# Kernel optimization log

Measured on AMD Instinct MI355X. Metric: run time of the kernel, lower is better.

Reference implementation:

```python
import jax, jax.numpy as jnp
import numpy as np

B, T, C = 2, 2048, 2048
H = 16
ROPE_DIM, NOPE_DIM, V_DIM = 64, 64, 128
HEAD_DIM = NOPE_DIM + ROPE_DIM  # 128
Q_RANK, KV_RANK = 1536, 512


def setup_inputs() -> dict:
    key = jax.random.key(0)
    ks = jax.random.split(key, 8)
    std = 0.02
    return {
        "x": jax.random.normal(ks[0], (B, T, C), jnp.float32),
        "cos": jax.random.normal(ks[1], (1, T, 1, ROPE_DIM // 2), jnp.float32),
        "sin": jax.random.normal(ks[2], (1, T, 1, ROPE_DIM // 2), jnp.float32),
        "wq_down": jax.random.normal(ks[3], (Q_RANK, C), jnp.float32) * std,
        "wq_up": jax.random.normal(ks[4], (H * HEAD_DIM, Q_RANK), jnp.float32) * std,
        "wkv_down": jax.random.normal(ks[5], (KV_RANK, C), jnp.float32) * std,
        "wkv_up": jax.random.normal(ks[6], (H * (HEAD_DIM + V_DIM), KV_RANK), jnp.float32) * std,
        "wo": jax.random.normal(ks[7], (C, H * V_DIM), jnp.float32) * std,
    }


def _rope(x, cos, sin):
    # x: [B, T, H, rope_dim]
    d = x.shape[-1] // 2
    x1, x2 = x[..., :d], x[..., d:]
    return jnp.concatenate([x1 * cos + x2 * sin, -x1 * sin + x2 * cos], axis=-1)


def _rms_norm(x):
    eps = jnp.finfo(x.dtype).eps
    return x * jax.lax.rsqrt(jnp.mean(jnp.square(x), axis=-1, keepdims=True) + eps)


def reference(x, cos, sin, wq_down, wq_up, wkv_down, wkv_up, wo):
    # Low-rank q projection
    q = jnp.einsum('btc,rc,dr->btd', x, wq_down, wq_up)
    q = q.reshape(B, T, H, HEAD_DIM)
    q_nope, q_rope = q[..., :NOPE_DIM], q[..., NOPE_DIM:]
    # Low-rank kv projection (naive decompression)
    kv = jnp.einsum('btc,rc,dr->btd', x, wkv_down, wkv_up)
    kv = kv.reshape(B, T, H, HEAD_DIM + V_DIM)
    k_nope = kv[..., :NOPE_DIM]
    k_rope = kv[..., NOPE_DIM:HEAD_DIM]
    v = kv[..., HEAD_DIM:]
    # Partial RoPE on the rope sub-dims only
    q_rope = _rope(q_rope, cos, sin)
    k_rope = _rope(k_rope, cos, sin)
    q = _rms_norm(jnp.concatenate([q_nope, q_rope], axis=-1))
    k = _rms_norm(jnp.concatenate([k_nope, k_rope], axis=-1))
    # Causal SDPA: [B, H, T, T]
    scale = 1.0 / jnp.sqrt(jnp.float32(HEAD_DIM))
    scores = jnp.einsum('bthd,bshd->bhts', q, k) * scale
    causal = jnp.tril(jnp.ones((T, T), dtype=bool))
    scores = jnp.where(causal, scores, jnp.finfo(scores.dtype).min)
    probs = jax.nn.softmax(scores, axis=-1)
    y = jnp.einsum('bhts,bshd->bthd', probs, v).reshape(B, T, H * V_DIM)
    return y @ wo.T
```

## Files before the change

kernel.cpp:

```cpp
#include <hip/hip_runtime.h>
#include <hip/hip_bf16.h>
#include <math.h>
#include <type_traits>

#define AS1 __attribute__((address_space(1)))
#define AS3 __attribute__((address_space(3)))

typedef __bf16  bf16x8 __attribute__((ext_vector_type(8)));
typedef float   f32x4  __attribute__((ext_vector_type(4)));
typedef __hip_bfloat16 bf16;

#define MFMA16x16x32 __builtin_amdgcn_mfma_f32_16x16x32_bf16

__device__ __forceinline__ void gload16(const void* g, void* l) {
  __builtin_amdgcn_global_load_lds((const AS1 void*)g, (AS3 void*)l, 16, 0, 0);
}

__device__ __forceinline__ unsigned short bfbits(float v) {
  return __builtin_bit_cast(unsigned short, __float2bfloat16(v));
}

#define LGKM0 __asm__ volatile("s_waitcnt lgkmcnt(0)" ::: "memory")
#define BARRIER __builtin_amdgcn_s_barrier()
#define VMCNT(n) __asm__ volatile("s_waitcnt vmcnt(" #n ")" ::: "memory")

struct CastArgs {
  const float4* src[6];
  ushort4* dst[6];
  unsigned bound[6];
};

__global__ __launch_bounds__(256) void f2bf_multi(CastArgs a) {
  unsigned i = blockIdx.x * 256 + threadIdx.x;
  if (i >= a.bound[5]) return;
  unsigned lo = 0;
  int s = 0;
#pragma unroll
  for (int k = 0; k < 5; k++) {
    if (i >= a.bound[k]) { s = k + 1; lo = a.bound[k]; }
  }
  unsigned idx = i - lo;
  float4 v = a.src[s][idx];
  ushort4 o;
  o.x = bfbits(v.x); o.y = bfbits(v.y); o.z = bfbits(v.z); o.w = bfbits(v.w);
  a.dst[s][idx] = o;
}

template <typename OutT, bool KVUP>
__global__ __launch_bounds__(512, 2) void gemm8p(const bf16* __restrict__ A,
                                                 const bf16* __restrict__ W,
                                                 OutT* __restrict__ Cp,
                                                 bf16* __restrict__ vT,
                                                 int N, int K, int lda) {
  __shared__ __align__(16) char lds[131072];
  const int t = threadIdx.x, w = t >> 6, lane = t & 63;
  const int quad = lane >> 4, l16 = lane & 15;
  const int wr = w >> 2, wc = w & 3;
  const size_t m0 = (size_t)blockIdx.x * 256;
  const size_t n0 = (size_t)blockIdx.y * 256;
  const int NI = K >> 7;

  const int srow = w * 8 + (lane >> 3);
  const int schunk = (lane & 7) ^ ((lane >> 3) & 7);
  const bf16* aS = A + (m0 + srow) * (size_t)lda + schunk * 8;
  const bf16* bS = W + (n0 + srow) * (size_t)K + schunk * 8;

  auto stageA = [&](int kt, int h) {
    const bf16* src = aS + (size_t)(h * 128) * lda + kt * 64;
    char* dst = lds + (kt & 1) * 32768 + h * 16384 + w * 1024;
    gload16(src, dst);
    gload16(src + (size_t)64 * lda, dst + 8192);
  };
  auto stageB = [&](int kt, int h) {
    const bf16* src = bS + (size_t)(h * 128) * K + kt * 64;
    char* dst = lds + 65536 + (kt & 1) * 32768 + h * 16384 + w * 1024;
    gload16(src, dst);
    gload16(src + (size_t)64 * K, dst + 8192);
  };

  const int cq0 = ((quad) ^ (l16 & 7)) * 16;
  const int cq1 = ((4 + quad) ^ (l16 & 7)) * 16;
  const char* aRb = lds + wr * 16384 + l16 * 128;
  const char* bRb = lds + 65536 + (wc >> 1) * 16384 + ((wc & 1) * 64 + l16) * 128;
  auto rdA = [&](int sl, int mf, int kh) -> bf16x8 {
    return *(const bf16x8*)(aRb + sl * 32768 + mf * 2048 + (kh ? cq1 : cq0));
  };
  auto rdB = [&](int sl, int nf, int kh) -> bf16x8 {
    return *(const bf16x8*)(bRb + sl * 32768 + nf * 2048 + (kh ? cq1 : cq0));
  };

  bf16x8 aR[8][2], bR[4][2];
  f32x4 acc[8][4];
#pragma unroll
  for (int i = 0; i < 8; i++)
#pragma unroll
    for (int j = 0; j < 4; j++) acc[i][j] = f32x4{0.f, 0.f, 0.f, 0.f};

  auto cluster = [&](int mh, int nh) {
    __builtin_amdgcn_s_setprio(1);
#pragma unroll
    for (int m2 = 0; m2 < 4; ++m2)
#pragma unroll
      for (int n2 = 0; n2 < 2; ++n2)
#pragma unroll
        for (int kh = 0; kh < 2; ++kh)
          acc[mh * 4 + m2][nh * 2 + n2] =
              MFMA16x16x32(aR[mh * 4 + m2][kh], bR[nh * 2 + n2][kh],
                           acc[mh * 4 + m2][nh * 2 + n2], 0, 0, 0);
    __builtin_amdgcn_s_setprio(0);
  };

  stageA(0, 0); stageA(0, 1); stageB(0, 0); stageB(0, 1);
  stageA(1, 0); stageA(1, 1); stageB(1, 0); stageB(1, 1);
  VMCNT(8);
  BARRIER;
#pragma unroll
  for (int mf = 0; mf < 4; ++mf)
#pragma unroll
    for (int kh = 0; kh < 2; ++kh) aR[mf][kh] = rdA(0, mf, kh);
#pragma unroll
  for (int nf = 0; nf < 2; ++nf)
#pragma unroll
    for (int kh = 0; kh < 2; ++kh) bR[nf][kh] = rdB(0, nf, kh);

  for (int i = 0; i < NI; ++i) {
    const int kt1 = 2 * i + 1, kt2 = 2 * i + 2, kt3 = 2 * i + 3;
    const bool hn = (i + 1 < NI);

#pragma unroll
    for (int kh = 0; kh < 2; ++kh) { bR[2][kh] = rdB(0, 2, kh); bR[3][kh] = rdB(0, 3, kh); }
    if (i > 0) stageB(kt1, 0);
    BARRIER; LGKM0;
    cluster(0, 0);
    BARRIER;

#pragma unroll
    for (int mf = 0; mf < 4; ++mf)
#pragma unroll
      for (int kh = 0; kh < 2; ++kh) aR[4 + mf][kh] = rdA(0, 4 + mf, kh);
    if (i > 0) stageB(kt1, 1);
    BARRIER; LGKM0;
    cluster(0, 1);
    BARRIER;

    if (hn) stageA(kt2, 0);
    BARRIER; LGKM0;
    cluster(1, 0);
    if (hn) { VMCNT(2); } else { VMCNT(0); }
    BARRIER;

#pragma unroll
    for (int mf = 0; mf < 4; ++mf)
#pragma unroll
      for (int kh = 0; kh < 2; ++kh) aR[mf][kh] = rdA(1, mf, kh);
#pragma unroll
    for (int nf = 0; nf < 2; ++nf)
#pragma unroll
      for (int kh = 0; kh < 2; ++kh) bR[nf][kh] = rdB(1, nf, kh);
    if (hn) stageA(kt2, 1);
    BARRIER; LGKM0;
    cluster(1, 1);
    BARRIER;

#pragma unroll
    for (int kh = 0; kh < 2; ++kh) { bR[2][kh] = rdB(1, 2, kh); bR[3][kh] = rdB(1, 3, kh); }
    if (hn) stageB(kt2, 0);
    BARRIER; LGKM0;
    cluster(0, 0);
    BARRIER;

#pragma unroll
    for (int mf = 0; mf < 4; ++mf)
#pragma unroll
      for (int kh = 0; kh < 2; ++kh) aR[4 + mf][kh] = rdA(1, 4 + mf, kh);
    if (hn) stageB(kt2, 1);
    BARRIER; LGKM0;
    cluster(0, 1);
    BARRIER;

    if (hn) stageA(kt3, 0);
    BARRIER; LGKM0;
    cluster(1, 0);
    if (hn) { VMCNT(2); }
    BARRIER;

    if (hn) {
#pragma unroll
      for (int mf = 0; mf < 4; ++mf)
#pragma unroll
        for (int kh = 0; kh < 2; ++kh) aR[mf][kh] = rdA(0, mf, kh);
#pragma unroll
      for (int nf = 0; nf < 2; ++nf)
#pragma unroll
        for (int kh = 0; kh < 2; ++kh) bR[nf][kh] = rdB(0, nf, kh);
      stageA(kt3, 1);
    }
    BARRIER; LGKM0;
    cluster(1, 1);
    BARRIER;
  }

  if constexpr (!KVUP) {
#pragma unroll
    for (int mf = 0; mf < 8; ++mf)
#pragma unroll
      for (int nf = 0; nf < 4; ++nf)
#pragma unroll
        for (int r = 0; r < 4; ++r) {
          size_t row = m0 + wr * 128 + mf * 16 + quad * 4 + r;
          size_t col = n0 + wc * 64 + nf * 16 + l16;
          float v = acc[mf][nf][r];
          if constexpr (std::is_same<OutT, float>::value)
            Cp[row * N + col] = v;
          else
            Cp[row * N + col] = __float2bfloat16(v);
        }
  } else {
    const int head = (int)(n0 >> 8);
    if (wc < 2) {
#pragma unroll
      for (int mf = 0; mf < 8; ++mf)
#pragma unroll
        for (int nf = 0; nf < 4; ++nf)
#pragma unroll
          for (int r = 0; r < 4; ++r) {
            size_t row = m0 + wr * 128 + mf * 16 + quad * 4 + r;
            size_t col = n0 + wc * 64 + nf * 16 + l16;
            Cp[row * 4096 + col] = __float2bfloat16(acc[mf][nf][r]);
          }
    } else {
#pragma unroll
      for (int mf = 0; mf < 8; ++mf) {
        size_t row = m0 + wr * 128 + mf * 16 + quad * 4;
        int bb = (int)(row >> 11), tloc = (int)(row & 2047);
#pragma unroll
        for (int nf = 0; nf < 4; ++nf) {
          int d = (wc - 2) * 64 + nf * 16 + l16;
          ushort4 v4;
          v4.x = bfbits(acc[mf][nf][0]);
          v4.y = bfbits(acc[mf][nf][1]);
          v4.z = bfbits(acc[mf][nf][2]);
          v4.w = bfbits(acc[mf][nf][3]);
          *(ushort4*)(vT + ((size_t)(bb * 16 + head) * 128 + d) * 2048 + tloc) = v4;
        }
      }
    }
  }
}

__global__ __launch_bounds__(256) void rope_rms(const bf16* __restrict__ qraw,
                                                const bf16* __restrict__ kvraw,
                                                const float* __restrict__ cosp,
                                                const float* __restrict__ sinp,
                                                bf16* __restrict__ qn,
                                                bf16* __restrict__ kn) {
  const int bt = blockIdx.x;
  const int w = threadIdx.x >> 6, lane = threadIdx.x & 63;
  const int h = blockIdx.y * 4 + w;
  const int tt = bt & 2047;
  const float c = cosp[tt * 32 + (lane & 31)];
  const float s = sinp[tt * 32 + (lane & 31)];
  const float inv128 = 1.0f / 128.0f;
  const float eps = 1.1920929e-7f;

  {
    const bf16* base = qraw + (size_t)bt * 2048 + h * 128;
    float a = (float)base[lane];
    float o = (float)base[64 + lane];
    float partner = __shfl_xor(o, 32);
    float orope = (lane < 32) ? (o * c + partner * s) : (o * c - partner * s);
    float ss = a * a + orope * orope;
#pragma unroll
    for (int off = 1; off < 64; off <<= 1) ss += __shfl_xor(ss, off);
    float rn = rsqrtf(ss * inv128 + eps);
    bf16* outp = qn + ((size_t)bt * 16 + h) * 128;
    outp[lane] = __float2bfloat16(a * rn);
    outp[64 + lane] = __float2bfloat16(orope * rn);
  }
  {
    const bf16* base = kvraw + (size_t)bt * 4096 + h * 256;
    float a = (float)base[lane];
    float o = (float)base[64 + lane];
    float partner = __shfl_xor(o, 32);
    float orope = (lane < 32) ? (o * c + partner * s) : (o * c - partner * s);
    float ss = a * a + orope * orope;
#pragma unroll
    for (int off = 1; off < 64; off <<= 1) ss += __shfl_xor(ss, off);
    float rn = rsqrtf(ss * inv128 + eps);
    bf16* outp = kn + ((size_t)bt * 16 + h) * 128;
    outp[lane] = __float2bfloat16(a * rn);
    outp[64 + lane] = __float2bfloat16(orope * rn);
  }
}

__global__ __launch_bounds__(256, 2) void attn_kernel(const bf16* __restrict__ qn,
                                                      const bf16* __restrict__ kn,
                                                      const bf16* __restrict__ vT,
                                                      bf16* __restrict__ y) {
  __shared__ __align__(16) bf16 Ks[2 * 64 * 128];
  __shared__ __align__(16) bf16 Vs[2 * 128 * 64];
  __shared__ __align__(16) bf16 Ps[4 * 16 * 64];
  const int t = threadIdx.x, w = t >> 6, lane = t & 63;
  const int quad = lane >> 4, l16 = lane & 15;
  const int b = blockIdx.x >> 4, h = blockIdx.x & 15;
  const int pr = (int)blockIdx.y;
  const int T_ = 2048, H_ = 16;
  const float K1 = 0.08838834764831845f * 1.4426950408889634f;
  const float K2 = -12.0f * 1.4426950408889634f;

  const int cgk = l16 ^ ((w * 4 + quad) & 7);
  const char* kg0 = (const char*)(kn + ((size_t)(b * T_) * H_ + h) * 128)
                    + (size_t)(w * 4 + quad) * 4096 + (size_t)cgk * 16;
  const int vrow = w * 8 + (lane >> 3);
  const int cgv = (lane & 7) ^ (vrow & 7);
  const char* vg0 = (const char*)(vT + ((size_t)(b * H_ + h) * 128 + vrow) * T_)
                    + (size_t)cgv * 16;

  auto stage = [&](auto bufc, int it2) {
    constexpr int BUF = decltype(bufc)::value;
    const size_t koff = (size_t)it2 * 262144;
    const size_t voff = (size_t)it2 * 128;
#pragma unroll
    for (int is = 0; is < 4; ++is)
      gload16(kg0 + koff + (size_t)is * 65536,
              (char*)Ks + BUF * 16384 + is * 4096 + w * 1024);
#pragma unroll
    for (int is = 0; is < 4; ++is)
      gload16(vg0 + voff + (size_t)is * 131072,
              (char*)Vs + BUF * 16384 + is * 4096 + w * 1024);
  };

  auto body = [&](auto bufc, int it, int nt, int xb,
                  bf16x8* qf, f32x4* yacc, float* lrow) {
    constexpr int BUF = decltype(bufc)::value;
    if (it + 1 < nt) {
      stage(std::integral_constant<int, 1 - BUF>{}, it + 1);
      __asm__ volatile("s_waitcnt vmcnt(8)" ::: "memory");
    } else {
      __asm__ volatile("s_waitcnt vmcnt(0)" ::: "memory");
    }
    __asm__ volatile("s_barrier" ::: "memory");

    f32x4 sacc[4];
#pragma unroll
    for (int cg = 0; cg < 4; cg++) sacc[cg] = f32x4{0.f, 0.f, 0.f, 0.f};
    __builtin_amdgcn_s_setprio(1);
#pragma unroll
    for (int cg = 0; cg < 4; ++cg) {
#pragma unroll
      for (int ks = 0; ks < 4; ++ks) {
        const int pos = (ks * 4 + quad) ^ (l16 & 7);
        const bf16x8 kf = *(const bf16x8*)((const char*)Ks + BUF * 16384 +
                                           (cg * 16 + l16) * 256 + pos * 16);
        sacc[cg] = MFMA16x16x32(qf[ks], kf, sacc[cg], 0, 0, 0);
      }
    }
    __builtin_amdgcn_s_setprio(0);

    const bool diag = (it == xb);
    float p[4][4];
#pragma unroll
    for (int cg = 0; cg < 4; ++cg)
#pragma unroll
      for (int r = 0; r < 4; ++r) {
        float e;
        if (diag && (cg * 16 + l16 > w * 16 + quad * 4 + r))
          e = 0.0f;
        else
          e = exp2f(fmaf(sacc[cg][r], K1, K2));
        p[cg][r] = e;
        lrow[r] += e;
      }

#pragma unroll
    for (int cg = 0; cg < 4; cg++)
#pragma unroll
      for (int r = 0; r < 4; r++) {
        const int row = quad * 4 + r;
        const int col = cg * 16 + l16;
        Ps[w * 1024 + row * 64 + (((col >> 3) ^ (row & 7)) << 3) + (col & 7)] =
            __float2bfloat16(p[cg][r]);
      }
    __asm__ volatile("s_waitcnt lgkmcnt(0)" ::: "memory");

    bf16x8 pf[2];
#pragma unroll
    for (int k2 = 0; k2 < 2; k2++)
      pf[k2] = *(const bf16x8*)(&Ps[w * 1024 + l16 * 64 +
                                    (((k2 * 4 + quad) ^ (l16 & 7)) << 3)]);
    __builtin_amdgcn_s_setprio(1);
#pragma unroll
    for (int dg = 0; dg < 8; dg++) {
#pragma unroll
      for (int k2 = 0; k2 < 2; k2++) {
        const int pos = (k2 * 4 + quad) ^ (l16 & 7);
        const bf16x8 vf = *(const bf16x8*)((const char*)Vs + BUF * 16384 +
                                           (dg * 16 + l16) * 128 + pos * 16);
        yacc[dg] = MFMA16x16x32(pf[k2], vf, yacc[dg], 0, 0, 0);
      }
    }
    __builtin_amdgcn_s_setprio(0);
    __asm__ volatile("s_barrier" ::: "memory");
  };

  const std::integral_constant<int, 0> c0{};
  const std::integral_constant<int, 1> c1{};

  for (int sidx = 0; sidx < 2; ++sidx) {
    const int xb = sidx ? pr : (31 - pr);
    const int q0 = xb * 64;
    const int nt = xb + 1;

    bf16x8 qf[4];
    {
      const bf16* qbase = qn + ((size_t)(b * T_ + q0 + w * 16 + l16) * H_ + h) * 128;
#pragma unroll
      for (int ks = 0; ks < 4; ks++) qf[ks] = *(const bf16x8*)(qbase + ks * 32 + quad * 8);
    }
    f32x4 yacc[8];
#pragma unroll
    for (int i = 0; i < 8; i++) yacc[i] = f32x4{0.f, 0.f, 0.f, 0.f};
    float lrow[4] = {0.f, 0.f, 0.f, 0.f};

    stage(c0, 0);
    int it = 0;
    for (; it + 2 <= nt; it += 2) {
      body(c0, it, nt, xb, qf, yacc, lrow);
      body(c1, it + 1, nt, xb, qf, yacc, lrow);
    }
    if (it < nt) body(c0, it, nt, xb, qf, yacc, lrow);

#pragma unroll
    for (int off = 1; off < 16; off <<= 1)
#pragma unroll
      for (int r = 0; r < 4; r++) lrow[r] += __shfl_xor(lrow[r], off);
#pragma unroll
    for (int r = 0; r < 4; r++) {
      float inv = 1.0f / lrow[r];
      size_t qrow = (size_t)(b * T_ + q0 + w * 16 + quad * 4 + r);
      bf16* outp = y + qrow * 2048 + h * 128;
#pragma unroll
      for (int dg = 0; dg < 8; dg++)
        outp[dg * 16 + l16] = __float2bfloat16(yacc[dg][r] * inv);
    }
  }
}

extern "C" void kernel_launch(void* const* d_in, const int* in_sizes, int n_in,
                              void* d_out, int out_size, void* d_ws, size_t ws_size,
                              hipStream_t stream) {
  (void)in_sizes; (void)n_in; (void)out_size; (void)ws_size;
  const float* x    = (const float*)d_in[0];
  const float* cosp = (const float*)d_in[1];
  const float* sinp = (const float*)d_in[2];
  const float* wqd  = (const float*)d_in[3];
  const float* wqu  = (const float*)d_in[4];
  const float* wkvd = (const float*)d_in[5];
  const float* wkvu = (const float*)d_in[6];
  const float* wo   = (const float*)d_in[7];
  float* out = (float*)d_out;

  char* ws = (char*)d_ws;
  size_t off = 0;
  auto alloc = [&](size_t elems) { bf16* p = (bf16*)(ws + off); off += elems * 2; return p; };
  bf16* xb      = alloc((size_t)4096 * 2048);
  bf16* wqdB    = alloc((size_t)1536 * 2048);
  bf16* wkvdB   = alloc((size_t)512 * 2048);
  bf16* wquB    = alloc((size_t)2048 * 1536);
  bf16* wkvuB   = alloc((size_t)4096 * 512);
  bf16* woB     = alloc((size_t)2048 * 2048);
  bf16* qkvdown = alloc((size_t)4096 * 2048);
  bf16* qraw    = alloc((size_t)4096 * 2048);
  bf16* kvraw   = alloc((size_t)4096 * 4096);
  bf16* qnb     = alloc((size_t)4096 * 16 * 128);
  bf16* knb     = alloc((size_t)4096 * 16 * 128);
  bf16* vTb     = alloc((size_t)2 * 16 * 128 * 2048);
  bf16* yb      = alloc((size_t)4096 * 2048);

  CastArgs ca;
  const float* srcs[6] = {x, wqd, wkvd, wqu, wkvu, wo};
  bf16* dsts[6]        = {xb, wqdB, wkvdB, wquB, wkvuB, woB};
  size_t cnts[6] = {(size_t)4096 * 2048, (size_t)1536 * 2048, (size_t)512 * 2048,
                    (size_t)2048 * 1536, (size_t)4096 * 512,  (size_t)2048 * 2048};
  unsigned cum = 0;
  for (int i = 0; i < 6; i++) {
    ca.src[i] = (const float4*)srcs[i];
    ca.dst[i] = (ushort4*)dsts[i];
    cum += (unsigned)(cnts[i] / 4);
    ca.bound[i] = cum;
  }
  f2bf_multi<<<dim3((cum + 255) / 256), 256, 0, stream>>>(ca);

  gemm8p<bf16, false><<<dim3(16, 8), 512, 0, stream>>>(
      xb, wqdB, qkvdown, nullptr, 2048, 2048, 2048);
  gemm8p<bf16, false><<<dim3(16, 8), 512, 0, stream>>>(
      qkvdown, wquB, qraw, nullptr, 2048, 1536, 2048);
  gemm8p<bf16, true><<<dim3(16, 16), 512, 0, stream>>>(
      qkvdown + 1536, wkvuB, kvraw, vTb, 4096, 512, 2048);
  rope_rms<<<dim3(4096, 4), 256, 0, stream>>>(qraw, kvraw, cosp, sinp, qnb, knb);
  attn_kernel<<<dim3(32, 16), 256, 0, stream>>>(qnb, knb, vTb, yb);
  gemm8p<float, false><<<dim3(16, 8), 512, 0, stream>>>(
      yb, woB, out, nullptr, 2048, 2048, 2048);
}
```

Measured before the change: 400.2 us.

## Split-K the q-down, q-up and output GEMMs with fp32 partial merge

```diff
diff --git a/kernel.cpp b/kernel.cpp
--- a/kernel.cpp
+++ b/kernel.cpp
@@ -46,24 +46,49 @@
   a.dst[s][idx] = o;
 }
 
-template <typename OutT, bool KVUP>
+template <typename OutT>
+__global__ __launch_bounds__(256) void addmerge(const float4* __restrict__ p0,
+                                                const float4* __restrict__ p1,
+                                                OutT* __restrict__ out, unsigned n4) {
+  for (unsigned i = blockIdx.x * 256 + threadIdx.x; i < n4; i += gridDim.x * 256) {
+    float4 a = p0[i], b = p1[i];
+    if constexpr (std::is_same<OutT, float>::value) {
+      float4 o;
+      o.x = a.x + b.x; o.y = a.y + b.y; o.z = a.z + b.z; o.w = a.w + b.w;
+      ((float4*)out)[i] = o;
+    } else {
+      ushort4 o;
+      o.x = bfbits(a.x + b.x); o.y = bfbits(a.y + b.y);
+      o.z = bfbits(a.z + b.z); o.w = bfbits(a.w + b.w);
+      ((ushort4*)out)[i] = o;
+    }
+  }
+}
+
+template <typename OutT, bool KVUP, bool SPLIT>
 __global__ __launch_bounds__(512, 2) void gemm8p(const bf16* __restrict__ A,
                                                  const bf16* __restrict__ W,
                                                  OutT* __restrict__ Cp,
                                                  bf16* __restrict__ vT,
-                                                 int N, int K, int lda) {
+                                                 float* __restrict__ pp0,
+                                                 float* __restrict__ pp1,
+                                                 int N, int Klen, int lda, int ldb) {
   __shared__ __align__(16) char lds[131072];
   const int t = threadIdx.x, w = t >> 6, lane = t & 63;
   const int quad = lane >> 4, l16 = lane & 15;
   const int wr = w >> 2, wc = w & 3;
   const size_t m0 = (size_t)blockIdx.x * 256;
   const size_t n0 = (size_t)blockIdx.y * 256;
-  const int NI = K >> 7;
+  if constexpr (SPLIT) {
+    const size_t zo = (size_t)blockIdx.z * Klen;
+    A += zo; W += zo;
+  }
+  const int NI = Klen >> 7;
 
   const int srow = w * 8 + (lane >> 3);
   const int schunk = (lane & 7) ^ ((lane >> 3) & 7);
   const bf16* aS = A + (m0 + srow) * (size_t)lda + schunk * 8;
-  const bf16* bS = W + (n0 + srow) * (size_t)K + schunk * 8;
+  const bf16* bS = W + (n0 + srow) * (size_t)ldb + schunk * 8;
 
   auto stageA = [&](int kt, int h) {
     const bf16* src = aS + (size_t)(h * 128) * lda + kt * 64;
@@ -72,10 +97,10 @@
     gload16(src + (size_t)64 * lda, dst + 8192);
   };
   auto stageB = [&](int kt, int h) {
-    const bf16* src = bS + (size_t)(h * 128) * K + kt * 64;
+    const bf16* src = bS + (size_t)(h * 128) * ldb + kt * 64;
     char* dst = lds + 65536 + (kt & 1) * 32768 + h * 16384 + w * 1024;
     gload16(src, dst);
-    gload16(src + (size_t)64 * K, dst + 8192);
+    gload16(src + (size_t)64 * ldb, dst + 8192);
   };
 
   const int cq0 = ((quad) ^ (l16 & 7)) * 16;
@@ -111,8 +136,8 @@
   };
 
   stageA(0, 0); stageA(0, 1); stageB(0, 0); stageB(0, 1);
-  stageA(1, 0); stageA(1, 1); stageB(1, 0); stageB(1, 1);
-  VMCNT(8);
+  stageB(1, 0); stageA(1, 0); stageB(1, 1);
+  VMCNT(6);
   BARRIER;
 #pragma unroll
   for (int mf = 0; mf < 4; ++mf)
@@ -129,7 +154,7 @@
 
 #pragma unroll
     for (int kh = 0; kh < 2; ++kh) { bR[2][kh] = rdB(0, 2, kh); bR[3][kh] = rdB(0, 3, kh); }
-    if (i > 0) stageB(kt1, 0);
+    stageA(kt1, 1);
     BARRIER; LGKM0;
     cluster(0, 0);
     BARRIER;
@@ -138,7 +163,7 @@
     for (int mf = 0; mf < 4; ++mf)
 #pragma unroll
       for (int kh = 0; kh < 2; ++kh) aR[4 + mf][kh] = rdA(0, 4 + mf, kh);
-    if (i > 0) stageB(kt1, 1);
+    if (hn) stageB(kt2, 0);
     BARRIER; LGKM0;
     cluster(0, 1);
     BARRIER;
@@ -146,7 +171,7 @@
     if (hn) stageA(kt2, 0);
     BARRIER; LGKM0;
     cluster(1, 0);
-    if (hn) { VMCNT(2); } else { VMCNT(0); }
+    if (hn) { VMCNT(4); } else { VMCNT(0); }
     BARRIER;
 
 #pragma unroll
@@ -157,50 +182,62 @@
     for (int nf = 0; nf < 2; ++nf)
 #pragma unroll
       for (int kh = 0; kh < 2; ++kh) bR[nf][kh] = rdB(1, nf, kh);
+    if (hn) stageB(kt2, 1);
+    BARRIER; LGKM0;
+    cluster(1, 1);
+    BARRIER;
+
+#pragma unroll
+    for (int kh = 0; kh < 2; ++kh) { bR[2][kh] = rdB(1, 2, kh); bR[3][kh] = rdB(1, 3, kh); }
     if (hn) stageA(kt2, 1);
     BARRIER; LGKM0;
+    cluster(0, 0);
+    BARRIER;
+
+#pragma unroll
+    for (int mf = 0; mf < 4; ++mf)
+#pragma unroll
+      for (int kh = 0; kh < 2; ++kh) aR[4 + mf][kh] = rdA(1, 4 + mf, kh);
+    if (hn) stageB(kt3, 0);
+    BARRIER; LGKM0;
+    cluster(0, 1);
+    BARRIER;
+
+    if (hn) stageA(kt3, 0);
+    BARRIER; LGKM0;
+    cluster(1, 0);
+    if (hn) { VMCNT(4); }
+    BARRIER;
+
+    if (hn) {
+#pragma unroll
+      for (int mf = 0; mf < 4; ++mf)
+#pragma unroll
+        for (int kh = 0; kh < 2; ++kh) aR[mf][kh] = rdA(0, mf, kh);
+#pragma unroll
+      for (int nf = 0; nf < 2; ++nf)
+#pragma unroll
+        for (int kh = 0; kh < 2; ++kh) bR[nf][kh] = rdB(0, nf, kh);
+      stageB(kt3, 1);
+    }
+    BARRIER; LGKM0;
     cluster(1, 1);
     BARRIER;
-
-#pragma unroll
-    for (int kh = 0; kh < 2; ++kh) { bR[2][kh] = rdB(1, 2, kh); bR[3][kh] = rdB(1, 3, kh); }
-    if (hn) stageB(kt2, 0);
-    BARRIER; LGKM0;
-    cluster(0, 0);
-    BARRIER;
-
-#pragma unroll
-    for (int mf = 0; mf < 4; ++mf)
-#pragma unroll
-      for (int kh = 0; kh < 2; ++kh) aR[4 + mf][kh] = rdA(1, 4 + mf, kh);
-    if (hn) stageB(kt2, 1);
-    BARRIER; LGKM0;
-    cluster(0, 1);
-    BARRIER;
-
-    if (hn) stageA(kt3, 0);
-    BARRIER; LGKM0;
-    cluster(1, 0);
-    if (hn) { VMCNT(2); }
-    BARRIER;
-
-    if (hn) {
-#pragma unroll
-      for (int mf = 0; mf < 4; ++mf)
-#pragma unroll
-        for (int kh = 0; kh < 2; ++kh) aR[mf][kh] = rdA(0, mf, kh);
-#pragma unroll
-      for (int nf = 0; nf < 2; ++nf)
-#pragma unroll
-        for (int kh = 0; kh < 2; ++kh) bR[nf][kh] = rdB(0, nf, kh);
-      stageA(kt3, 1);
-    }
-    BARRIER; LGKM0;
-    cluster(1, 1);
-    BARRIER;
-  }
-
-  if constexpr (!KVUP) {
+  }
+
+  if constexpr (SPLIT) {
+    float* dst = blockIdx.z ? pp1 : pp0;
+#pragma unroll
+    for (int mf = 0; mf < 8; ++mf)
+#pragma unroll
+      for (int nf = 0; nf < 4; ++nf)
+#pragma unroll
+        for (int r = 0; r < 4; ++r) {
+          size_t row = m0 + wr * 128 + mf * 16 + quad * 4 + r;
+          size_t col = n0 + wc * 64 + nf * 16 + l16;
+          dst[row * N + col] = acc[mf][nf][r];
+        }
+  } else if constexpr (!KVUP) {
 #pragma unroll
     for (int mf = 0; mf < 8; ++mf)
 #pragma unroll
@@ -477,6 +514,9 @@
   bf16* vTb     = alloc((size_t)2 * 16 * 128 * 2048);
   bf16* yb      = alloc((size_t)4096 * 2048);
 
+  float* pp0 = (float*)kvraw;
+  float* pp1 = (float*)qnb;
+
   CastArgs ca;
   const float* srcs[6] = {x, wqd, wkvd, wqu, wkvu, wo};
   bf16* dsts[6]        = {xb, wqdB, wkvdB, wquB, wkvuB, woB};
@@ -491,14 +531,22 @@
   }
   f2bf_multi<<<dim3((cum + 255) / 256), 256, 0, stream>>>(ca);
 
-  gemm8p<bf16, false><<<dim3(16, 8), 512, 0, stream>>>(
-      xb, wqdB, qkvdown, nullptr, 2048, 2048, 2048);
-  gemm8p<bf16, false><<<dim3(16, 8), 512, 0, stream>>>(
-      qkvdown, wquB, qraw, nullptr, 2048, 1536, 2048);
-  gemm8p<bf16, true><<<dim3(16, 16), 512, 0, stream>>>(
-      qkvdown + 1536, wkvuB, kvraw, vTb, 4096, 512, 2048);
+  const unsigned n4 = (unsigned)((size_t)4096 * 2048 / 4);
+
+  gemm8p<float, false, true><<<dim3(16, 8, 2), 512, 0, stream>>>(
+      xb, wqdB, (float*)nullptr, nullptr, pp0, pp1, 2048, 1024, 2048, 2048);
+  addmerge<bf16><<<dim3(2048), 256, 0, stream>>>((const float4*)pp0, (const float4*)pp1,
+                                                 qkvdown, n4);
+  gemm8p<float, false, true><<<dim3(16, 8, 2), 512, 0, stream>>>(
+      qkvdown, wquB, (float*)nullptr, nullptr, pp0, pp1, 2048, 768, 2048, 1536);
+  addmerge<bf16><<<dim3(2048), 256, 0, stream>>>((const float4*)pp0, (const float4*)pp1,
+                                                 qraw, n4);
+  gemm8p<bf16, true, false><<<dim3(16, 16), 512, 0, stream>>>(
+      qkvdown + 1536, wkvuB, kvraw, vTb, nullptr, nullptr, 4096, 512, 2048, 512);
   rope_rms<<<dim3(4096, 4), 256, 0, stream>>>(qraw, kvraw, cosp, sinp, qnb, knb);
   attn_kernel<<<dim3(32, 16), 256, 0, stream>>>(qnb, knb, vTb, yb);
-  gemm8p<float, false><<<dim3(16, 8), 512, 0, stream>>>(
-      yb, woB, out, nullptr, 2048, 2048, 2048);
-}
+  gemm8p<float, false, true><<<dim3(16, 8, 2), 512, 0, stream>>>(
+      yb, woB, (float*)nullptr, nullptr, pp0, pp1, 2048, 1024, 2048, 2048);
+  addmerge<float><<<dim3(2048), 256, 0, stream>>>((const float4*)pp0, (const float4*)pp1,
+                                                  out, n4);
+}
```

Result: no change. 397.1 us (-0.8%).
